# Performance work log

Measured on AMD Instinct MI355X. Metric: run time of the kernel, lower is better.

## Reference

```python
import jax, jax.numpy as jnp
import numpy as np

N_NODES = 100000
N_EDGES = 1600000
D_IN = 64
D_HID = 64


def setup_inputs() -> dict:
    key = jax.random.key(0)
    k1, k2, k3, k4, k5 = jax.random.split(key, 5)
    x = jax.random.normal(k1, (N_NODES, D_IN), dtype=jnp.float32)
    edge_index = jax.random.randint(k2, (2, N_EDGES), 0, N_NODES, dtype=jnp.int64)
    edge_weight = jax.random.uniform(k3, (N_EDGES,), dtype=jnp.float32)
    # GCNConv glorot-initialized linear weights (bias=False)
    s0 = (6.0 / (D_IN + D_HID)) ** 0.5
    W0 = jax.random.uniform(k4, (D_IN, D_HID), minval=-s0, maxval=s0, dtype=jnp.float32)
    s1 = (6.0 / (D_HID + D_HID)) ** 0.5
    W1 = jax.random.uniform(k5, (D_HID, D_HID), minval=-s1, maxval=s1, dtype=jnp.float32)
    return {"x": x, "edge_index": edge_index, "edge_weight": edge_weight, "W0": W0, "W1": W1}


def _gcn_layer(x, W, src, dst, edge_weight, deg_inv_sqrt, n_nodes):
    # h = X W  (bias=False)
    h = x @ W  # [N, D]
    # symmetric normalization including self-loops (weight 1)
    norm = deg_inv_sqrt[src] * edge_weight * deg_inv_sqrt[dst]  # [E]
    # gather src features, scale, scatter-sum at dst
    agg = jax.ops.segment_sum(norm[:, None] * h[src], dst, num_segments=n_nodes)
    # self-loop contribution: norm_ii = deg_inv_sqrt[i]^2 * 1
    agg = agg + (deg_inv_sqrt * deg_inv_sqrt)[:, None] * h
    return jax.nn.relu(agg)  # dropout is identity in eval mode


def reference(x, edge_index, edge_weight, W0, W1):
    src, dst = edge_index[0], edge_index[1]
    # degree with self-loops (self-loop weight = 1), aggregated at dst (source_to_target flow)
    deg = jax.ops.segment_sum(edge_weight, dst, num_segments=N_NODES) + 1.0
    deg_inv_sqrt = jax.lax.rsqrt(deg)
    x = _gcn_layer(x, W0, src, dst, edge_weight, deg_inv_sqrt, N_NODES)
    x = _gcn_layer(x, W1, src, dst, edge_weight, deg_inv_sqrt, N_NODES)
    return x
```

## Files before the change

kernel.cpp:

```cpp
#include <hip/hip_runtime.h>
#include <hip/hip_fp16.h>

#define D 64
#define BSH 9
#define BSZ (1 << BSH)
#define PB 2048
#define CAP 18432
#define SCAP 9216

__global__ __launch_bounds__(256) void initcur(int* __restrict__ ccur, int nbuck) {
    int t = threadIdx.x;
    if (t < nbuck) ccur[t] = t * CAP;
}

__global__ __launch_bounds__(512) void bucket1(const int* __restrict__ src,
                                               const int* __restrict__ dst,
                                               const float* __restrict__ ew,
                                               int* __restrict__ ccur,
                                               int2* __restrict__ pairs,
                                               int E, int nbuck) {
    __shared__ int hist[512];
    __shared__ int lbase[512];
    __shared__ int gbase[512];
    __shared__ int w0s[PB];
    __shared__ int w1s[PB];
    __shared__ unsigned short bids[PB];
    int t = threadIdx.x;
    hist[t] = 0;
    __syncthreads();
    int e0 = blockIdx.x * PB;
    int cnt = min(PB, E - e0);
    int b[4], lr[4], w0[4], w1[4];
    int i4 = t * 4;
    bool full4 = (i4 + 4 <= cnt);
    if (full4) {
        int4   s4 = *(const int4*)&src[e0 + i4];
        int4   d4 = *(const int4*)&dst[e0 + i4];
        float4 w4 = *(const float4*)&ew[e0 + i4];
        int ss[4] = {s4.x, s4.y, s4.z, s4.w};
        int ds[4] = {d4.x, d4.y, d4.z, d4.w};
        float wv[4] = {w4.x, w4.y, w4.z, w4.w};
#pragma unroll
        for (int k = 0; k < 4; ++k) {
            b[k]  = ds[k] >> BSH;
            w0[k] = ss[k] | ((ds[k] & (BSZ - 1)) << 17);
            w1[k] = __float_as_int(wv[k]);
            lr[k] = atomicAdd(&hist[b[k]], 1);
        }
    } else {
#pragma unroll
        for (int k = 0; k < 4; ++k) {
            int idx = i4 + k;
            if (idx < cnt) {
                int d = dst[e0 + idx];
                b[k]  = d >> BSH;
                w0[k] = src[e0 + idx] | ((d & (BSZ - 1)) << 17);
                w1[k] = __float_as_int(ew[e0 + idx]);
                lr[k] = atomicAdd(&hist[b[k]], 1);
            }
        }
    }
    __syncthreads();
    int hv = hist[t];
    lbase[t] = hv;
    __syncthreads();
    for (int off = 1; off < 512; off <<= 1) {
        int u = (t >= off) ? lbase[t - off] : 0;
        __syncthreads();
        lbase[t] += u;
        __syncthreads();
    }
    int excl = lbase[t] - hv;
    __syncthreads();
    lbase[t] = excl;
    if (t < nbuck && hv > 0) gbase[t] = atomicAdd(&ccur[t], hv);
    __syncthreads();
#pragma unroll
    for (int k = 0; k < 4; ++k) {
        int idx = i4 + k;
        if (idx < cnt) {
            int slot = lbase[b[k]] + lr[k];
            w0s[slot] = w0[k];
            w1s[slot] = w1[k];
            bids[slot] = (unsigned short)b[k];
        }
    }
    __syncthreads();
    for (int i = t; i < cnt; i += 512) {
        int bb = bids[i];
        int pos = gbase[bb] + (i - lbase[bb]);
        pairs[pos] = make_int2(w0s[i], w1s[i]);
    }
}

__global__ __launch_bounds__(512) void sort2(int2* __restrict__ pairs,
                                             const int* __restrict__ ccur,
                                             int* __restrict__ offsets,
                                             int* __restrict__ ends,
                                             float* __restrict__ dis,
                                             int N, int nbuck) {
    __shared__ int2 se[SCAP];
    __shared__ int cnt[512];
    __shared__ float sdeg[512];
    __shared__ int lb[512];
    __shared__ int cur[512];
    int b = blockIdx.x;
    int t = threadIdx.x;
    int base = b * CAP;
    int cntb = min(ccur[b] - base, SCAP);
    for (int i = t; i < cntb; i += 512) se[i] = pairs[base + i];
    cnt[t] = 0;
    sdeg[t] = 0.0f;
    __syncthreads();
    for (int i = t; i < cntb; i += 512) {
        int2 p = se[i];
        int dl = p.x >> 17;
        atomicAdd(&cnt[dl], 1);
        atomicAdd(&sdeg[dl], __int_as_float(p.y));
    }
    __syncthreads();
    int node = (b << BSH) + t;
    int pc = (node < N) ? ((cnt[t] + 1 + 31) & ~31) : 0;
    lb[t] = pc;
    __syncthreads();
    for (int off = 1; off < 512; off <<= 1) {
        int u = (t >= off) ? lb[t - off] : 0;
        __syncthreads();
        lb[t] += u;
        __syncthreads();
    }
    int excl = lb[t] - pc;
    float dloc = rsqrtf(sdeg[t] + 1.0f);
    __syncthreads();
    sdeg[t] = dloc;
    cur[t]  = base + excl;
    int myend = base + excl + pc;
    if (node < N) {
        offsets[node] = base + excl;
        ends[node]    = myend;
        dis[node]     = dloc;
    }
    __syncthreads();
    for (int i = t; i < cntb; i += 512) {
        int2 p = se[i];
        int dl = p.x >> 17;
        int s  = p.x & 0x1FFFF;
        int pos = atomicAdd(&cur[dl], 1);
        float w = __int_as_float(p.y) * sdeg[dl];
        pairs[pos] = make_int2(s, __float_as_int(w));
    }
    __syncthreads();
    if (node < N) {
        int c = cur[t];
        pairs[c] = make_int2(node, __float_as_int(dloc));
        for (int i = c + 1; i < myend; ++i) pairs[i] = make_int2(0, 0);
    }
}

__global__ __launch_bounds__(256) void gemm64h(const float* __restrict__ X,
                                               const float* __restrict__ W,
                                               const float* __restrict__ dis,
                                               __half* __restrict__ Hb, int n) {
    __shared__ float Ws[64 * 64];
    __shared__ float Xs[16 * 64];
    for (int t = threadIdx.x; t < 64 * 64; t += 256) Ws[t] = W[t];
    int row0 = blockIdx.x * 16;
    for (int t = threadIdx.x; t < 16 * 64; t += 256) {
        int r = row0 + (t >> 6);
        Xs[t] = (r < n) ? X[r * 64 + (t & 63)] : 0.0f;
    }
    __syncthreads();
    int r  = threadIdx.x >> 4;
    int jc = (threadIdx.x & 15) * 4;
    float4 acc = make_float4(0.f, 0.f, 0.f, 0.f);
#pragma unroll
    for (int k = 0; k < 64; ++k) {
        float xv = Xs[r * 64 + k];
        float4 w = *(const float4*)&Ws[k * 64 + jc];
        acc.x += xv * w.x; acc.y += xv * w.y; acc.z += xv * w.z; acc.w += xv * w.w;
    }
    int rr = row0 + r;
    if (rr < n) {
        float ds = dis[rr];
        ushort4 pk;
        pk.x = __half_as_ushort(__float2half(ds * acc.x));
        pk.y = __half_as_ushort(__float2half(ds * acc.y));
        pk.z = __half_as_ushort(__float2half(ds * acc.z));
        pk.w = __half_as_ushort(__float2half(ds * acc.w));
        *(ushort4*)&Hb[rr * 64 + jc] = pk;
    }
}

__global__ __launch_bounds__(256) void gather64(const int2* __restrict__ pairs,
                                                const int* __restrict__ offsets,
                                                const int* __restrict__ ends,
                                                const __half* __restrict__ Hb,
                                                float* __restrict__ OUT, int N) {
    int node = blockIdx.x * 4 + (threadIdx.x >> 6);
    if (node >= N) return;
    int lane = threadIdx.x & 63;
    int g    = lane >> 3;
    int fl   = (lane & 7) * 8;
    int beg = offsets[node];
    int end = ends[node];
    __half2 z = __float2half2_rn(0.0f);
    __half2 a0[4] = {z, z, z, z};
    __half2 a1[4] = {z, z, z, z};
    __half2 a2[4] = {z, z, z, z};
    __half2 a3[4] = {z, z, z, z};
    for (int e = beg; e < end; e += 32) {
        int2 p0 = pairs[e + g];
        int2 p1 = pairs[e + 8 + g];
        int2 p2 = pairs[e + 16 + g];
        int2 p3 = pairs[e + 24 + g];
        uint4 r0 = *(const uint4*)(Hb + (size_t)p0.x * 64 + fl);
        uint4 r1 = *(const uint4*)(Hb + (size_t)p1.x * 64 + fl);
        uint4 r2 = *(const uint4*)(Hb + (size_t)p2.x * 64 + fl);
        uint4 r3 = *(const uint4*)(Hb + (size_t)p3.x * 64 + fl);
        __half2 w0 = __half2half2(__float2half(__int_as_float(p0.y)));
        __half2 w1 = __half2half2(__float2half(__int_as_float(p1.y)));
        __half2 w2 = __half2half2(__float2half(__int_as_float(p2.y)));
        __half2 w3 = __half2half2(__float2half(__int_as_float(p3.y)));
        const __half2* h0 = (const __half2*)&r0;
        const __half2* h1 = (const __half2*)&r1;
        const __half2* h2 = (const __half2*)&r2;
        const __half2* h3 = (const __half2*)&r3;
#pragma unroll
        for (int k = 0; k < 4; ++k) {
            a0[k] = __hfma2(w0, h0[k], a0[k]);
            a1[k] = __hfma2(w1, h1[k], a1[k]);
            a2[k] = __hfma2(w2, h2[k], a2[k]);
            a3[k] = __hfma2(w3, h3[k], a3[k]);
        }
    }
    __half2 a[4];
#pragma unroll
    for (int k = 0; k < 4; ++k)
        a[k] = __hadd2(__hadd2(a0[k], a1[k]), __hadd2(a2[k], a3[k]));
#pragma unroll
    for (int m = 8; m < 64; m <<= 1) {
#pragma unroll
        for (int k = 0; k < 4; ++k) {
            unsigned u = __shfl_xor(*(unsigned*)&a[k], m, 64);
            a[k] = __hadd2(a[k], *(__half2*)&u);
        }
    }
    if (g < 2) {
        int o = g * 2;
        float2 f0 = __half22float2(a[o]);
        float2 f1 = __half22float2(a[o + 1]);
        float4 vv;
        vv.x = fmaxf(f0.x, 0.0f);
        vv.y = fmaxf(f0.y, 0.0f);
        vv.z = fmaxf(f1.x, 0.0f);
        vv.w = fmaxf(f1.y, 0.0f);
        *(float4*)&OUT[node * 64 + fl + g * 4] = vv;
    }
}

extern "C" void kernel_launch(void* const* d_in, const int* in_sizes, int n_in,
                              void* d_out, int out_size, void* d_ws, size_t ws_size,
                              hipStream_t stream) {
    const float* x  = (const float*)d_in[0];
    const int*   ei = (const int*)d_in[1];
    const float* ew = (const float*)d_in[2];
    const float* W0 = (const float*)d_in[3];
    const float* W1 = (const float*)d_in[4];
    float* out = (float*)d_out;

    const int N = in_sizes[0] / D;
    const int E = in_sizes[2];
    const int* src = ei;
    const int* dst = ei + E;

    const int nbuck = (N + BSZ - 1) >> BSH;
    const int Na = (N + 1 + 255) & ~255;

    float* dis     = (float*)d_ws;
    int*   offsets = (int*)d_ws + Na;
    int*   ends    = (int*)d_ws + 2 * Na;
    int*   ccur    = (int*)d_ws + 3 * Na;
    int2*  pairs   = (int2*)((int*)d_ws + 3 * Na + 1024);
    __half* Hb     = (__half*)(pairs + (size_t)nbuck * CAP);

    const int nb1 = (E + PB - 1) / PB;

    initcur<<<1, 256, 0, stream>>>(ccur, nbuck);
    bucket1<<<nb1, 512, 0, stream>>>(src, dst, ew, ccur, pairs, E, nbuck);
    sort2<<<nbuck, 512, 0, stream>>>(pairs, ccur, offsets, ends, dis, N, nbuck);

    const int gemm_grid   = (N + 15) / 16;
    const int gather_grid = (N + 3) / 4;

    gemm64h<<<gemm_grid, 256, 0, stream>>>(x, W0, dis, Hb, N);
    gather64<<<gather_grid, 256, 0, stream>>>(pairs, offsets, ends, Hb, out, N);

    gemm64h<<<gemm_grid, 256, 0, stream>>>(out, W1, dis, Hb, N);
    gather64<<<gather_grid, 256, 0, stream>>>(pairs, offsets, ends, Hb, out, N);
}
```

Measured before the change: 212.1 us.

## Pack edge entries into 32-bit words and double bucketing chunk size

Each sorted edge entry is now packed into one 32-bit word: a 17-bit source index plus a 15-bit positive half-precision weight with the sign and lowest mantissa bit dropped. Each gather lane loads one word and broadcasts it with wave shuffles, which halves the edge-list traffic in both aggregation passes. Offsets and ends are merged into one int2 range array, and padding is now zeroed by all threads in parallel. The bucketing kernel handles 4096 edges per block with 8 per thread and stores bucket ids as bytes. The cost is reduced weight precision, and the packing only works while node indices fit in 17 bits and weights stay non-negative.

```diff
diff --git a/kernel.cpp b/kernel.cpp
--- a/kernel.cpp
+++ b/kernel.cpp
@@ -4,44 +4,48 @@
 #define D 64
 #define BSH 9
 #define BSZ (1 << BSH)
-#define PB 2048
-#define CAP 18432
+#define PB 4096
+#define CAPR 18432
+#define CAPU (2 * CAPR)
 #define SCAP 9216
 
 __global__ __launch_bounds__(256) void initcur(int* __restrict__ ccur, int nbuck) {
     int t = threadIdx.x;
-    if (t < nbuck) ccur[t] = t * CAP;
+    if (t < nbuck) ccur[t] = t * CAPR;
 }
 
 __global__ __launch_bounds__(512) void bucket1(const int* __restrict__ src,
                                                const int* __restrict__ dst,
                                                const float* __restrict__ ew,
                                                int* __restrict__ ccur,
-                                               int2* __restrict__ pairs,
+                                               int2* __restrict__ pairs2,
                                                int E, int nbuck) {
     __shared__ int hist[512];
     __shared__ int lbase[512];
     __shared__ int gbase[512];
     __shared__ int w0s[PB];
     __shared__ int w1s[PB];
-    __shared__ unsigned short bids[PB];
+    __shared__ unsigned char bids[PB];
     int t = threadIdx.x;
     hist[t] = 0;
     __syncthreads();
     int e0 = blockIdx.x * PB;
     int cnt = min(PB, E - e0);
-    int b[4], lr[4], w0[4], w1[4];
-    int i4 = t * 4;
-    bool full4 = (i4 + 4 <= cnt);
-    if (full4) {
-        int4   s4 = *(const int4*)&src[e0 + i4];
-        int4   d4 = *(const int4*)&dst[e0 + i4];
-        float4 w4 = *(const float4*)&ew[e0 + i4];
-        int ss[4] = {s4.x, s4.y, s4.z, s4.w};
-        int ds[4] = {d4.x, d4.y, d4.z, d4.w};
-        float wv[4] = {w4.x, w4.y, w4.z, w4.w};
-#pragma unroll
-        for (int k = 0; k < 4; ++k) {
+    int b[8], lr[8], w0[8], w1[8];
+    int i8 = t * 8;
+    bool full8 = (i8 + 8 <= cnt);
+    if (full8) {
+        int4   sa = *(const int4*)&src[e0 + i8];
+        int4   sb = *(const int4*)&src[e0 + i8 + 4];
+        int4   da = *(const int4*)&dst[e0 + i8];
+        int4   db = *(const int4*)&dst[e0 + i8 + 4];
+        float4 wa = *(const float4*)&ew[e0 + i8];
+        float4 wb = *(const float4*)&ew[e0 + i8 + 4];
+        int ss[8] = {sa.x, sa.y, sa.z, sa.w, sb.x, sb.y, sb.z, sb.w};
+        int ds[8] = {da.x, da.y, da.z, da.w, db.x, db.y, db.z, db.w};
+        float wv[8] = {wa.x, wa.y, wa.z, wa.w, wb.x, wb.y, wb.z, wb.w};
+#pragma unroll
+        for (int k = 0; k < 8; ++k) {
             b[k]  = ds[k] >> BSH;
             w0[k] = ss[k] | ((ds[k] & (BSZ - 1)) << 17);
             w1[k] = __float_as_int(wv[k]);
@@ -49,8 +53,8 @@
         }
     } else {
 #pragma unroll
-        for (int k = 0; k < 4; ++k) {
-            int idx = i4 + k;
+        for (int k = 0; k < 8; ++k) {
+            int idx = i8 + k;
             if (idx < cnt) {
                 int d = dst[e0 + idx];
                 b[k]  = d >> BSH;
@@ -76,27 +80,27 @@
     if (t < nbuck && hv > 0) gbase[t] = atomicAdd(&ccur[t], hv);
     __syncthreads();
 #pragma unroll
-    for (int k = 0; k < 4; ++k) {
-        int idx = i4 + k;
+    for (int k = 0; k < 8; ++k) {
+        int idx = i8 + k;
         if (idx < cnt) {
             int slot = lbase[b[k]] + lr[k];
             w0s[slot] = w0[k];
             w1s[slot] = w1[k];
-            bids[slot] = (unsigned short)b[k];
+            bids[slot] = (unsigned char)b[k];
         }
     }
     __syncthreads();
     for (int i = t; i < cnt; i += 512) {
         int bb = bids[i];
         int pos = gbase[bb] + (i - lbase[bb]);
-        pairs[pos] = make_int2(w0s[i], w1s[i]);
-    }
-}
-
-__global__ __launch_bounds__(512) void sort2(int2* __restrict__ pairs,
+        pairs2[pos] = make_int2(w0s[i], w1s[i]);
+    }
+}
+
+__global__ __launch_bounds__(512) void sort2(int2* __restrict__ pairs2,
+                                             unsigned int* __restrict__ pairsU,
                                              const int* __restrict__ ccur,
-                                             int* __restrict__ offsets,
-                                             int* __restrict__ ends,
+                                             int2* __restrict__ rng,
                                              float* __restrict__ dis,
                                              int N, int nbuck) {
     __shared__ int2 se[SCAP];
@@ -106,9 +110,10 @@
     __shared__ int cur[512];
     int b = blockIdx.x;
     int t = threadIdx.x;
-    int base = b * CAP;
-    int cntb = min(ccur[b] - base, SCAP);
-    for (int i = t; i < cntb; i += 512) se[i] = pairs[base + i];
+    int baseR = b * CAPR;
+    int baseU = b * CAPU;
+    int cntb = min(ccur[b] - baseR, SCAP);
+    for (int i = t; i < cntb; i += 512) se[i] = pairs2[baseR + i];
     cnt[t] = 0;
     sdeg[t] = 0.0f;
     __syncthreads();
@@ -130,16 +135,16 @@
         __syncthreads();
     }
     int excl = lb[t] - pc;
+    int totalPad = lb[511];
     float dloc = rsqrtf(sdeg[t] + 1.0f);
     __syncthreads();
     sdeg[t] = dloc;
-    cur[t]  = base + excl;
-    int myend = base + excl + pc;
+    cur[t]  = baseU + excl;
     if (node < N) {
-        offsets[node] = base + excl;
-        ends[node]    = myend;
-        dis[node]     = dloc;
-    }
+        rng[node] = make_int2(baseU + excl, baseU + excl + pc);
+        dis[node] = dloc;
+    }
+    for (int i = t; i < totalPad; i += 512) pairsU[baseU + i] = 0u;
     __syncthreads();
     for (int i = t; i < cntb; i += 512) {
         int2 p = se[i];
@@ -147,13 +152,13 @@
         int s  = p.x & 0x1FFFF;
         int pos = atomicAdd(&cur[dl], 1);
         float w = __int_as_float(p.y) * sdeg[dl];
-        pairs[pos] = make_int2(s, __float_as_int(w));
+        unsigned int h = (unsigned int)__half_as_ushort(__float2half_rn(w));
+        pairsU[pos] = ((unsigned int)s << 15) | ((h + 1u) >> 1);
     }
     __syncthreads();
     if (node < N) {
-        int c = cur[t];
-        pairs[c] = make_int2(node, __float_as_int(dloc));
-        for (int i = c + 1; i < myend; ++i) pairs[i] = make_int2(0, 0);
+        unsigned int h = (unsigned int)__half_as_ushort(__float2half_rn(dloc));
+        pairsU[cur[t]] = ((unsigned int)node << 15) | ((h + 1u) >> 1);
     }
 }
 
@@ -191,9 +196,8 @@
     }
 }
 
-__global__ __launch_bounds__(256) void gather64(const int2* __restrict__ pairs,
-                                                const int* __restrict__ offsets,
-                                                const int* __restrict__ ends,
+__global__ __launch_bounds__(256) void gather64(const unsigned int* __restrict__ pairs,
+                                                const int2* __restrict__ rng,
                                                 const __half* __restrict__ Hb,
                                                 float* __restrict__ OUT, int N) {
     int node = blockIdx.x * 4 + (threadIdx.x >> 6);
@@ -201,26 +205,26 @@
     int lane = threadIdx.x & 63;
     int g    = lane >> 3;
     int fl   = (lane & 7) * 8;
-    int beg = offsets[node];
-    int end = ends[node];
+    int2 be = rng[node];
     __half2 z = __float2half2_rn(0.0f);
     __half2 a0[4] = {z, z, z, z};
     __half2 a1[4] = {z, z, z, z};
     __half2 a2[4] = {z, z, z, z};
     __half2 a3[4] = {z, z, z, z};
-    for (int e = beg; e < end; e += 32) {
-        int2 p0 = pairs[e + g];
-        int2 p1 = pairs[e + 8 + g];
-        int2 p2 = pairs[e + 16 + g];
-        int2 p3 = pairs[e + 24 + g];
-        uint4 r0 = *(const uint4*)(Hb + (size_t)p0.x * 64 + fl);
-        uint4 r1 = *(const uint4*)(Hb + (size_t)p1.x * 64 + fl);
-        uint4 r2 = *(const uint4*)(Hb + (size_t)p2.x * 64 + fl);
-        uint4 r3 = *(const uint4*)(Hb + (size_t)p3.x * 64 + fl);
-        __half2 w0 = __half2half2(__float2half(__int_as_float(p0.y)));
-        __half2 w1 = __half2half2(__float2half(__int_as_float(p1.y)));
-        __half2 w2 = __half2half2(__float2half(__int_as_float(p2.y)));
-        __half2 w3 = __half2half2(__float2half(__int_as_float(p3.y)));
+    for (int e = be.x; e < be.y; e += 32) {
+        unsigned int pv = pairs[e + (lane & 31)];
+        unsigned int q0 = __shfl(pv, g, 64);
+        unsigned int q1 = __shfl(pv, g + 8, 64);
+        unsigned int q2 = __shfl(pv, g + 16, 64);
+        unsigned int q3 = __shfl(pv, g + 24, 64);
+        uint4 r0 = *(const uint4*)(Hb + (size_t)(q0 >> 15) * 64 + fl);
+        uint4 r1 = *(const uint4*)(Hb + (size_t)(q1 >> 15) * 64 + fl);
+        uint4 r2 = *(const uint4*)(Hb + (size_t)(q2 >> 15) * 64 + fl);
+        uint4 r3 = *(const uint4*)(Hb + (size_t)(q3 >> 15) * 64 + fl);
+        __half2 w0 = __half2half2(__ushort_as_half((unsigned short)((q0 & 0x7FFFu) << 1)));
+        __half2 w1 = __half2half2(__ushort_as_half((unsigned short)((q1 & 0x7FFFu) << 1)));
+        __half2 w2 = __half2half2(__ushort_as_half((unsigned short)((q2 & 0x7FFFu) << 1)));
+        __half2 w3 = __half2half2(__ushort_as_half((unsigned short)((q3 & 0x7FFFu) << 1)));
         const __half2* h0 = (const __half2*)&r0;
         const __half2* h1 = (const __half2*)&r1;
         const __half2* h2 = (const __half2*)&r2;
@@ -277,24 +281,24 @@
     const int Na = (N + 1 + 255) & ~255;
 
     float* dis     = (float*)d_ws;
-    int*   offsets = (int*)d_ws + Na;
-    int*   ends    = (int*)d_ws + 2 * Na;
+    int2*  rng     = (int2*)((int*)d_ws + Na);
     int*   ccur    = (int*)d_ws + 3 * Na;
-    int2*  pairs   = (int2*)((int*)d_ws + 3 * Na + 1024);
-    __half* Hb     = (__half*)(pairs + (size_t)nbuck * CAP);
+    int2*  pairs2  = (int2*)((int*)d_ws + 3 * Na + 1024);
+    unsigned int* pairsU = (unsigned int*)pairs2;
+    __half* Hb     = (__half*)((int*)d_ws + 3 * Na + 1024 + (size_t)nbuck * CAPU);
 
     const int nb1 = (E + PB - 1) / PB;
 
     initcur<<<1, 256, 0, stream>>>(ccur, nbuck);
-    bucket1<<<nb1, 512, 0, stream>>>(src, dst, ew, ccur, pairs, E, nbuck);
-    sort2<<<nbuck, 512, 0, stream>>>(pairs, ccur, offsets, ends, dis, N, nbuck);
+    bucket1<<<nb1, 512, 0, stream>>>(src, dst, ew, ccur, pairs2, E, nbuck);
+    sort2<<<nbuck, 512, 0, stream>>>(pairs2, pairsU, ccur, rng, dis, N, nbuck);
 
     const int gemm_grid   = (N + 15) / 16;
     const int gather_grid = (N + 3) / 4;
 
     gemm64h<<<gemm_grid, 256, 0, stream>>>(x, W0, dis, Hb, N);
-    gather64<<<gather_grid, 256, 0, stream>>>(pairs, offsets, ends, Hb, out, N);
+    gather64<<<gather_grid, 256, 0, stream>>>(pairsU, rng, Hb, out, N);
 
     gemm64h<<<gemm_grid, 256, 0, stream>>>(out, W1, dis, Hb, N);
-    gather64<<<gather_grid, 256, 0, stream>>>(pairs, offsets, ends, Hb, out, N);
-}
+    gather64<<<gather_grid, 256, 0, stream>>>(pairsU, rng, Hb, out, N);
+}
```

Result: faster. 195.7 us (-7.7%).
